# Kernel optimization log

Hardware: AMD Instinct MI355X
Metric: run time of the kernel (lower is better)

The kernel has to match this reference:

```python
import jax, jax.numpy as jnp
import numpy as np

HIDDEN = 2048
NUM_HEADS = 16
HEAD_DIM = HIDDEN // NUM_HEADS


def setup_inputs() -> dict:
    key = jax.random.key(0)
    k1, k2, k3 = jax.random.split(key, 3)
    B, S = 2, 2048
    hidden_states = jax.random.normal(k1, (B, S, HIDDEN), dtype=jnp.float32)
    attention_mask = jnp.zeros((B, 1, 1, S), dtype=jnp.float32)
    W_qkv = jax.random.normal(k2, (HIDDEN, 3 * HIDDEN), dtype=jnp.float32) * (1.0 / np.sqrt(HIDDEN))
    b_qkv = jnp.zeros((3 * HIDDEN,), dtype=jnp.float32)
    W_out = jax.random.normal(k3, (HIDDEN, HIDDEN), dtype=jnp.float32) * (1.0 / np.sqrt(HIDDEN))
    b_out = jnp.zeros((HIDDEN,), dtype=jnp.float32)
    return {"hidden_states": hidden_states, "attention_mask": attention_mask,
            "W_qkv": W_qkv, "b_qkv": b_qkv, "W_out": W_out, "b_out": b_out}


def reference(hidden_states, attention_mask, W_qkv, b_qkv, W_out, b_out):
    B, S, H = hidden_states.shape
    scale = 1.0 / np.sqrt(HEAD_DIM)
    # fused QKV projection (column-parallel linear, world_size=1)
    mixed = hidden_states @ W_qkv + b_qkv                      # [B,S,3H]
    q, k, v = jnp.split(mixed, 3, axis=-1)
    # [B, heads, S, head_dim]
    q = q.reshape(B, S, NUM_HEADS, HEAD_DIM).transpose(0, 2, 1, 3)
    k = k.reshape(B, S, NUM_HEADS, HEAD_DIM).transpose(0, 2, 1, 3)
    v = v.reshape(B, S, NUM_HEADS, HEAD_DIM).transpose(0, 2, 1, 3)
    scores = jnp.einsum('bhqd,bhkd->bhqk', q, k) * scale       # [B,h,S,S]
    scores = scores + attention_mask                            # additive mask broadcast
    probs = jax.nn.softmax(scores, axis=-1)
    ctx = jnp.einsum('bhqk,bhkd->bhqd', probs, v)               # [B,h,S,d]
    ctx = ctx.transpose(0, 2, 1, 3).reshape(B, S, H)
    return ctx @ W_out + b_out
```

## Files before the change

### kernel.cpp

```cpp
#include <hip/hip_runtime.h>
#include <hip/hip_bf16.h>
#include <stdint.h>

typedef __attribute__((ext_vector_type(4)))  float   f32x4;
typedef __attribute__((ext_vector_type(16))) float   f32x16;
typedef __attribute__((ext_vector_type(8)))  __bf16  bf16x8;
typedef __attribute__((ext_vector_type(8)))  short   s16x8;
typedef __attribute__((ext_vector_type(4)))  unsigned short u16x4;
typedef __attribute__((ext_vector_type(4)))  float   fl4;
typedef __attribute__((ext_vector_type(2)))  unsigned int u32x2;
typedef __attribute__((ext_vector_type(4)))  unsigned int u32x4;

#define DEVFN static __device__ __forceinline__

constexpr int BATCH = 2, SEQ = 2048, HID = 2048, NHEAD = 16, HDIM = 128;
constexpr int MROWS = BATCH * SEQ;
constexpr int N3    = 3 * HID;
constexpr float LOG2E = 1.44269504088896340736f;
constexpr float SCALE_LOG2E = 0.12751649736170852f;
constexpr float DEFER_THR = 11.541560327111708f;

DEVFN unsigned short f2bf(float f) {
  unsigned int u = __float_as_uint(f);
  u += 0x7FFFu + ((u >> 16) & 1u);
  return (unsigned short)(u >> 16);
}
DEVFN float bf2f(unsigned short h) { return __uint_as_float(((unsigned int)h) << 16); }

DEVFN void async_cp16(const void* g, void* l) {
  __builtin_amdgcn_global_load_lds(
      (__attribute__((address_space(1))) void*)g,
      (__attribute__((address_space(3))) void*)l, 16, 0, 0);
}

DEVFN f32x4 mfma_bf16(bf16x8 a, bf16x8 b, f32x4 c) {
  return __builtin_amdgcn_mfma_f32_16x16x32_bf16(a, b, c, 0, 0, 0);
}
DEVFN f32x16 mfma32(bf16x8 a, bf16x8 b, f32x16 c) {
  return __builtin_amdgcn_mfma_f32_32x32x16_bf16(a, b, c, 0, 0, 0);
}
DEVFN unsigned cvt_pk_bf16(float lo, float hi) {
  unsigned r;
  asm("v_cvt_pk_bf16_f32 %0, %1, %2" : "=v"(r) : "v"(lo), "v"(hi));
  return r;
}

__global__ __launch_bounds__(256) void cvt_bf16(const float* __restrict__ x,
                                                unsigned short* __restrict__ hi, int n4) {
  for (int i = blockIdx.x * blockDim.x + threadIdx.x; i < n4; i += gridDim.x * blockDim.x) {
    fl4 v = ((const fl4*)x)[i];
    u16x4 h;
#pragma unroll
    for (int j = 0; j < 4; j++) h[j] = f2bf(v[j]);
    ((u16x4*)hi)[i] = h;
  }
}

__global__ __launch_bounds__(256) void cvt_transpose(const float* __restrict__ W,
                                                     unsigned short* __restrict__ T,
                                                     int R, int C) {
  __shared__ float tile[32][33];
  const int c0 = blockIdx.x * 32, r0 = blockIdx.y * 32;
  const int tx = threadIdx.x, ty = threadIdx.y;
#pragma unroll
  for (int i = 0; i < 4; i++) tile[ty + 8 * i][tx] = W[(size_t)(r0 + ty + 8 * i) * C + c0 + tx];
  __syncthreads();
#pragma unroll
  for (int i = 0; i < 4; i++) {
    const float v = tile[tx][ty + 8 * i];
    T[(size_t)(c0 + ty + 8 * i) * R + r0 + tx] = f2bf(v);
  }
}

template <bool OUT_BF16>
__global__ __launch_bounds__(512, 1) void gemm_ring(const unsigned short* __restrict__ A,
                                                    const unsigned short* __restrict__ Bt,
                                                    const float* __restrict__ bias,
                                                    void* __restrict__ Cout, int Ndim) {
  constexpr int KDIM  = 2048;
  constexpr int NT    = KDIM / 64;
  constexpr int ASLOT = 256 * 64;
  constexpr int BSLOT = 128 * 64;
  constexpr int SLOT  = ASLOT + BSLOT;
  __shared__ __align__(16) unsigned short smem[3 * SLOT];

  const int tid = threadIdx.x;
  const int wid = tid >> 6, lane = tid & 63;
  const int wm = wid >> 2, wn = wid & 3;
  const int g = lane >> 4, q = lane & 15;
  const int n0 = blockIdx.x * 128, m0 = blockIdx.y * 256;

  const int srow = (wid << 3) + (lane >> 3);
  const int scol = (((lane & 7) ^ (lane >> 3)) << 4);
  const char* gA = (const char*)A  + ((size_t)(m0 + srow) * KDIM) * 2 + scol;
  const char* gB = (const char*)Bt + ((size_t)(n0 + srow) * KDIM) * 2 + scol;
  const int dbase = ((wid << 3)) << 7;

  f32x4 acc[8][2] = {};
  const int axor = (q & 7) << 4;

  auto STAGE = [&](int tt, int slot) {
    char* sA = (char*)(smem + slot * SLOT);
    char* sB = (char*)(smem + slot * SLOT + ASLOT);
    const size_t koff = (size_t)tt << 7;
#pragma unroll
    for (int i = 0; i < 4; i++)
      async_cp16(gA + (size_t)(i * 64) * (KDIM * 2) + koff, sA + dbase + (i << 13));
#pragma unroll
    for (int i = 0; i < 2; i++)
      async_cp16(gB + (size_t)(i * 64) * (KDIM * 2) + koff, sB + dbase + (i << 13));
  };

  auto COMPUTE = [&](int slot) {
    const char* sA = (const char*)(smem + slot * SLOT);
    const char* sB = (const char*)(smem + slot * SLOT + ASLOT);
#pragma unroll
    for (int ks = 0; ks < 2; ks++) {
      const int kb = (ks << 6) + (g << 4);
      bf16x8 av[8], bv[2];
#pragma unroll
      for (int nf = 0; nf < 2; nf++) {
        const int row = (wn << 5) + (nf << 4) + q;
        bv[nf] = *(const bf16x8*)(sB + (row << 7) + (kb ^ axor));
      }
#pragma unroll
      for (int mf = 0; mf < 8; mf++) {
        const int row = (wm << 7) + (mf << 4) + q;
        av[mf] = *(const bf16x8*)(sA + (row << 7) + (kb ^ axor));
      }
#pragma unroll
      for (int mf = 0; mf < 8; mf++)
#pragma unroll
        for (int nf = 0; nf < 2; nf++)
          acc[mf][nf] = mfma_bf16(av[mf], bv[nf], acc[mf][nf]);
    }
  };

  STAGE(0, 0);
  STAGE(1, 1);
  int s2 = 2, sc = 0;
#pragma unroll 1
  for (int t = 0; t < NT - 2; ++t) {
    asm volatile("s_waitcnt vmcnt(6)" ::: "memory");
    __builtin_amdgcn_s_barrier();
    asm volatile("" ::: "memory");
    STAGE(t + 2, s2);
    COMPUTE(sc);
    s2 = (s2 == 2) ? 0 : s2 + 1;
    sc = (sc == 2) ? 0 : sc + 1;
  }
  asm volatile("s_waitcnt vmcnt(6)" ::: "memory");
  __builtin_amdgcn_s_barrier();
  asm volatile("" ::: "memory");
  COMPUTE(sc);
  sc = (sc == 2) ? 0 : sc + 1;
  asm volatile("s_waitcnt vmcnt(0)" ::: "memory");
  __builtin_amdgcn_s_barrier();
  asm volatile("" ::: "memory");
  COMPUTE(sc);

  float bvv[2];
#pragma unroll
  for (int nf = 0; nf < 2; nf++) bvv[nf] = bias[n0 + (wn << 5) + (nf << 4) + q];
#pragma unroll
  for (int mf = 0; mf < 8; mf++) {
    const int rowg = m0 + (wm << 7) + (mf << 4) + (g << 2);
#pragma unroll
    for (int nf = 0; nf < 2; nf++) {
      const int colg = n0 + (wn << 5) + (nf << 4) + q;
#pragma unroll
      for (int r = 0; r < 4; r++) {
        const float v = acc[mf][nf][r] + bvv[nf];
        if (OUT_BF16)
          ((unsigned short*)Cout)[(size_t)(rowg + r) * Ndim + colg] = f2bf(v);
        else
          ((float*)Cout)[(size_t)(rowg + r) * Ndim + colg] = v;
      }
    }
  }
}

__global__ __launch_bounds__(256) void transpose_v(const unsigned short* __restrict__ qkv,
                                                   unsigned short* __restrict__ vt) {
  __shared__ __align__(16) unsigned short tile[64][136];
  const int z = blockIdx.y, b = z >> 4, h = z & 15;
  const int s0 = blockIdx.x << 6;
  const int t = threadIdx.x;
#pragma unroll
  for (int i = 0; i < 4; i++) {
    const int idx = t + (i << 8);
    const int row = idx >> 4, ch = idx & 15;
    *(s16x8*)&tile[row][ch << 3] =
        *(const s16x8*)(qkv + (size_t)(b * SEQ + s0 + row) * N3 + 2 * HID + h * HDIM + (ch << 3));
  }
  __syncthreads();
#pragma unroll
  for (int i = 0; i < 4; i++) {
    const int idx = t + (i << 8);
    const int d = idx >> 3, sc = idx & 7;
    s16x8 v;
#pragma unroll
    for (int j = 0; j < 8; j++) v[j] = (short)tile[(sc << 3) + j][d];
    *(s16x8*)(vt + (size_t)(z * HDIM + d) * SEQ + s0 + (sc << 3)) = v;
  }
}

__global__ __launch_bounds__(512, 2) void attn_kernel(const unsigned short* __restrict__ qkv,
                                                      const unsigned short* __restrict__ vt,
                                                      const float* __restrict__ mask,
                                                      unsigned short* __restrict__ ctx) {
  constexpr int NT    = SEQ / 64;
  constexpr int KSLOT = 64 * 128;
  constexpr int VSLOT = 128 * 64;
  constexpr int SLOT  = KSLOT + VSLOT;
  __shared__ __align__(16) unsigned short sKV[3 * SLOT];
  __shared__ __align__(16) float sM[SEQ];

  const int bid = blockIdx.x;
  const int z  = ((bid & 7) << 2) + ((bid >> 3) >> 3);
  const int qb = (bid >> 3) & 7;
  const int b = z >> 4, h = z & 15;
  const int tid = threadIdx.x, wid = tid >> 6, lane = tid & 63;
  const int l31 = lane & 31, hi = lane >> 5;
  const int q0w = (qb << 8) + (wid << 5);

  {
    fl4 m = ((const fl4*)(mask + (size_t)b * SEQ))[tid];
    m *= LOG2E;
    ((fl4*)sM)[tid] = m;
  }

  bf16x8 bq[8];
  {
    const char* qrow = (const char*)(qkv + (size_t)(b * SEQ + q0w + l31) * N3 + h * HDIM);
#pragma unroll
    for (int kc = 0; kc < 8; kc++) bq[kc] = *(const bf16x8*)(qrow + (kc << 5) + (hi << 4));
  }

  f32x16 acc2[4] = {};
  float mrun = -1e30f, lrun = 0.f;

  const char* gK = (const char*)qkv + ((size_t)(b * SEQ) * N3 + HID + h * HDIM) * 2;
  const char* gV = (const char*)vt + ((size_t)z * HDIM * SEQ) * 2;

  auto STAGE = [&](int tt, int slot) {
    char* base = (char*)(sKV + slot * SLOT);
    const int k0 = tt << 6;
#pragma unroll
    for (int i = 0; i < 2; i++) {
      const int krow = (i << 5) + (tid >> 4);
      const int kc = (((tid & 15) << 4)) ^ ((krow & 7) << 4);
      async_cp16(gK + ((size_t)(k0 + krow) * N3) * 2 + kc, base + (i << 13) + (wid << 10));
    }
#pragma unroll
    for (int i = 0; i < 2; i++) {
      const int vrow = (i << 6) + (tid >> 3);
      const int vc = (((tid & 7) << 4)) ^ ((vrow & 7) << 4);
      async_cp16(gV + ((size_t)vrow * SEQ + k0) * 2 + vc,
                 base + (KSLOT * 2) + (i << 13) + (wid << 10));
    }
  };

  auto COMPUTE = [&](int t, int slot) {
    const char* sK = (const char*)(sKV + slot * SLOT);
    const char* sV = (const char*)(sKV + slot * SLOT + KSLOT);
    const int k0 = t << 6;

    f32x16 accs[2] = {};
    __builtin_amdgcn_s_setprio(1);
#pragma unroll
    for (int kb = 0; kb < 2; kb++)
#pragma unroll
      for (int kc = 0; kc < 8; kc++) {
        const bf16x8 ka = *(const bf16x8*)(sK + (((kb << 5) + l31) << 8) +
                                           (((kc << 5) + (hi << 4)) ^ ((l31 & 7) << 4)));
        accs[kb] = mfma32(ka, bq[kc], accs[kb]);
      }
    __builtin_amdgcn_s_setprio(0);

    float p_[2][16];
#pragma unroll
    for (int kb = 0; kb < 2; kb++) {
      fl4 mk[4];
#pragma unroll
      for (int m = 0; m < 4; m++) mk[m] = *(const fl4*)&sM[k0 + (kb << 5) + (m << 3) + (hi << 2)];
#pragma unroll
      for (int r = 0; r < 16; r++)
        p_[kb][r] = fmaf(accs[kb][r], SCALE_LOG2E, mk[r >> 2][r & 3]);
    }
    float mt = p_[0][0];
#pragma unroll
    for (int kb = 0; kb < 2; kb++)
#pragma unroll
      for (int r = 0; r < 16; r++) mt = fmaxf(mt, p_[kb][r]);
    mt = fmaxf(mt, __shfl_xor(mt, 32));
    if (!__all(mt <= mrun + DEFER_THR)) {
      const float mnew = fmaxf(mrun, mt);
      const float fs = exp2f(mrun - mnew);
      lrun *= fs;
#pragma unroll
      for (int r = 0; r < 16; r++) {
        const int qr = (r & 3) + ((r >> 2) << 3) + (hi << 2);
        const float fr = __shfl(fs, (lane & 32) | qr);
#pragma unroll
        for (int db = 0; db < 4; db++) acc2[db][r] *= fr;
      }
      mrun = mnew;
    }
    float ps = 0.f;
#pragma unroll
    for (int kb = 0; kb < 2; kb++)
#pragma unroll
      for (int r = 0; r < 16; r++) {
        const float e = exp2f(p_[kb][r] - mrun);
        p_[kb][r] = e;
        ps += e;
      }
    ps += __shfl_xor(ps, 32);
    lrun += ps;

    bf16x8 pa[4];
#pragma unroll
    for (int kb = 0; kb < 2; kb++)
#pragma unroll
      for (int hh = 0; hh < 2; hh++) {
        const float* pp = &p_[kb][hh << 3];
        const unsigned x01 = cvt_pk_bf16(pp[0], pp[1]);
        const unsigned x23 = cvt_pk_bf16(pp[2], pp[3]);
        const unsigned y01 = cvt_pk_bf16(pp[4], pp[5]);
        const unsigned y23 = cvt_pk_bf16(pp[6], pp[7]);
        const u32x2 sa = __builtin_amdgcn_permlane32_swap(x01, y01, false, false);
        const u32x2 sb = __builtin_amdgcn_permlane32_swap(x23, y23, false, false);
        const u32x4 w = {sa[0], sb[0], sa[1], sb[1]};
        pa[(kb << 1) + hh] = __builtin_bit_cast(bf16x8, w);
      }

    __builtin_amdgcn_s_setprio(1);
#pragma unroll
    for (int db = 0; db < 4; db++)
#pragma unroll
      for (int ks = 0; ks < 4; ks++) {
        const bf16x8 bv = *(const bf16x8*)(sV + (((db << 5) + l31) << 7) +
                                           (((ks << 5) + (hi << 4)) ^ ((l31 & 7) << 4)));
        acc2[db] = mfma32(pa[ks], bv, acc2[db]);
      }
    __builtin_amdgcn_s_setprio(0);
  };

  STAGE(0, 0);
  STAGE(1, 1);
  __syncthreads();
  int s2 = 2, sc = 0;
#pragma unroll 1
  for (int t = 0; t < NT - 2; ++t) {
    asm volatile("s_waitcnt vmcnt(4)" ::: "memory");
    __builtin_amdgcn_s_barrier();
    asm volatile("" ::: "memory");
    STAGE(t + 2, s2);
    COMPUTE(t, sc);
    s2 = (s2 == 2) ? 0 : s2 + 1;
    sc = (sc == 2) ? 0 : sc + 1;
  }
  asm volatile("s_waitcnt vmcnt(4)" ::: "memory");
  __builtin_amdgcn_s_barrier();
  asm volatile("" ::: "memory");
  COMPUTE(NT - 2, sc);
  sc = (sc == 2) ? 0 : sc + 1;
  asm volatile("s_waitcnt vmcnt(0)" ::: "memory");
  __builtin_amdgcn_s_barrier();
  asm volatile("" ::: "memory");
  COMPUTE(NT - 1, sc);

  const float inv = 1.f / lrun;
#pragma unroll
  for (int r = 0; r < 16; r++) {
    const int qr = (r & 3) + ((r >> 2) << 3) + (hi << 2);
    const float fr = __shfl(inv, (lane & 32) | qr);
    unsigned short* crow = ctx + (size_t)(b * SEQ + q0w + qr) * HID + h * HDIM + l31;
#pragma unroll
    for (int db = 0; db < 4; db++) crow[db << 5] = f2bf(acc2[db][r] * fr);
  }
}

extern "C" void kernel_launch(void* const* d_in, const int* in_sizes, int n_in,
                              void* d_out, int out_size, void* d_ws, size_t ws_size,
                              hipStream_t stream) {
  const float* hs   = (const float*)d_in[0];
  const float* mask = (const float*)d_in[1];
  const float* Wqkv = (const float*)d_in[2];
  const float* bqkv = (const float*)d_in[3];
  const float* Wout = (const float*)d_in[4];
  const float* bout = (const float*)d_in[5];

  char* ws = (char*)d_ws;
  size_t off = 0;
  auto alloc = [&](size_t n) { char* p = ws + off; off += (n + 255) & ~(size_t)255; return p; };
  unsigned short* hs_bf = (unsigned short*)alloc((size_t)MROWS * HID * 2);
  unsigned short* wq_bf = (unsigned short*)alloc((size_t)N3 * HID * 2);
  unsigned short* wo_bf = (unsigned short*)alloc((size_t)HID * HID * 2);
  unsigned short* qkvb  = (unsigned short*)alloc((size_t)MROWS * N3 * 2);
  unsigned short* vtb   = (unsigned short*)alloc((size_t)BATCH * NHEAD * HDIM * SEQ * 2);
  unsigned short* ctxb  = (unsigned short*)alloc((size_t)MROWS * HID * 2);
  (void)ws_size;

  cvt_bf16<<<2048, 256, 0, stream>>>(hs, hs_bf, MROWS * HID / 4);
  dim3 tb(32, 8);
  cvt_transpose<<<dim3(N3 / 32, HID / 32), tb, 0, stream>>>(Wqkv, wq_bf, HID, N3);
  cvt_transpose<<<dim3(HID / 32, HID / 32), tb, 0, stream>>>(Wout, wo_bf, HID, HID);
  gemm_ring<true ><<<dim3(N3 / 128, MROWS / 256), 512, 0, stream>>>(hs_bf, wq_bf, bqkv, qkvb, N3);
  transpose_v<<<dim3(SEQ / 64, BATCH * NHEAD), 256, 0, stream>>>(qkvb, vtb);
  attn_kernel<<<256, 512, 0, stream>>>(qkvb, vtb, mask, ctxb);
  gemm_ring<false><<<dim3(HID / 128, MROWS / 256), 512, 0, stream>>>(ctxb, wo_bf, bout, (float*)d_out, HID);
}
```

Before: 268.9 us.

## Shrink attention blocks to 4 waves with double-buffered KV and new LDS swizzle

The attention kernel now uses 256-thread blocks covering 128 query rows (512 blocks instead of 256). The 3-slot KV ring becomes a double buffer, and the wait-for-all-loads plus barrier moves to the end of each iteration. The K/V LDS layout is reorganised with a 16-way XOR swizzle, and V is stored as two 64-row halves. The aim is more blocks and lower LDS use per block, so more blocks fit per CU and the tail is balanced better, at the cost of re-reading K/V twice as often and a shallower prefetch pipeline.

```diff
diff --git a/kernel.cpp b/kernel.cpp
--- a/kernel.cpp
+++ b/kernel.cpp
@@ -25,7 +25,6 @@
   u += 0x7FFFu + ((u >> 16) & 1u);
   return (unsigned short)(u >> 16);
 }
-DEVFN float bf2f(unsigned short h) { return __uint_as_float(((unsigned int)h) << 16); }
 
 DEVFN void async_cp16(const void* g, void* l) {
   __builtin_amdgcn_global_load_lds(
@@ -205,29 +204,31 @@
   }
 }
 
-__global__ __launch_bounds__(512, 2) void attn_kernel(const unsigned short* __restrict__ qkv,
+__global__ __launch_bounds__(256, 2) void attn_kernel(const unsigned short* __restrict__ qkv,
                                                       const unsigned short* __restrict__ vt,
                                                       const float* __restrict__ mask,
                                                       unsigned short* __restrict__ ctx) {
   constexpr int NT    = SEQ / 64;
   constexpr int KSLOT = 64 * 128;
-  constexpr int VSLOT = 128 * 64;
+  constexpr int VSLOT = 64 * 128;
   constexpr int SLOT  = KSLOT + VSLOT;
-  __shared__ __align__(16) unsigned short sKV[3 * SLOT];
+  __shared__ __align__(16) unsigned short sKV[2 * SLOT];
   __shared__ __align__(16) float sM[SEQ];
 
   const int bid = blockIdx.x;
-  const int z  = ((bid & 7) << 2) + ((bid >> 3) >> 3);
-  const int qb = (bid >> 3) & 7;
+  const int idx = bid >> 3;
+  const int z  = ((bid & 7) << 2) + (idx >> 4);
+  const int qb = idx & 15;
   const int b = z >> 4, h = z & 15;
   const int tid = threadIdx.x, wid = tid >> 6, lane = tid & 63;
   const int l31 = lane & 31, hi = lane >> 5;
-  const int q0w = (qb << 8) + (wid << 5);
-
-  {
-    fl4 m = ((const fl4*)(mask + (size_t)b * SEQ))[tid];
+  const int q0w = (qb << 7) + (wid << 5);
+
+#pragma unroll
+  for (int j = 0; j < 2; j++) {
+    fl4 m = ((const fl4*)(mask + (size_t)b * SEQ))[tid + (j << 8)];
     m *= LOG2E;
-    ((fl4*)sM)[tid] = m;
+    ((fl4*)sM)[tid + (j << 8)] = m;
   }
 
   bf16x8 bq[8];
@@ -244,20 +245,20 @@
   const char* gV = (const char*)vt + ((size_t)z * HDIM * SEQ) * 2;
 
   auto STAGE = [&](int tt, int slot) {
-    char* base = (char*)(sKV + slot * SLOT);
+    char* kb_ = (char*)(sKV + slot * SLOT);
+    char* vb_ = kb_ + KSLOT * 2;
     const int k0 = tt << 6;
 #pragma unroll
-    for (int i = 0; i < 2; i++) {
-      const int krow = (i << 5) + (tid >> 4);
-      const int kc = (((tid & 15) << 4)) ^ ((krow & 7) << 4);
-      async_cp16(gK + ((size_t)(k0 + krow) * N3) * 2 + kc, base + (i << 13) + (wid << 10));
-    }
-#pragma unroll
-    for (int i = 0; i < 2; i++) {
-      const int vrow = (i << 6) + (tid >> 3);
-      const int vc = (((tid & 7) << 4)) ^ ((vrow & 7) << 4);
-      async_cp16(gV + ((size_t)vrow * SEQ + k0) * 2 + vc,
-                 base + (KSLOT * 2) + (i << 13) + (wid << 10));
+    for (int i = 0; i < 4; i++) {
+      const int row = (i << 4) + (wid << 2) + (lane >> 4);
+      const int sl  = lane & 15;
+      const int dst = (i << 12) + (wid << 10);
+      async_cp16(gK + ((size_t)(k0 + row) * N3) * 2 + (((sl ^ (row & 15))) << 4),
+                 kb_ + dst);
+      const int sv  = sl ^ (row & 15);
+      const int dhi = sv >> 3, kc8 = sv & 7;
+      async_cp16(gV + ((size_t)((dhi << 6) + row) * SEQ + k0 + (kc8 << 3)) * 2,
+                 vb_ + dst);
     }
   };
 
@@ -272,8 +273,9 @@
     for (int kb = 0; kb < 2; kb++)
 #pragma unroll
       for (int kc = 0; kc < 8; kc++) {
-        const bf16x8 ka = *(const bf16x8*)(sK + (((kb << 5) + l31) << 8) +
-                                           (((kc << 5) + (hi << 4)) ^ ((l31 & 7) << 4)));
+        const int key = (kb << 5) + l31;
+        const bf16x8 ka = *(const bf16x8*)(sK + (key << 8) +
+                                           ((((kc << 1) + hi) ^ (l31 & 15)) << 4));
         accs[kb] = mfma32(ka, bq[kc], accs[kb]);
       }
     __builtin_amdgcn_s_setprio(0);
@@ -337,39 +339,29 @@
 
     __builtin_amdgcn_s_setprio(1);
 #pragma unroll
-    for (int db = 0; db < 4; db++)
+    for (int db = 0; db < 4; db++) {
+      const int dd = ((db & 1) << 5) + l31;
 #pragma unroll
       for (int ks = 0; ks < 4; ks++) {
-        const bf16x8 bv = *(const bf16x8*)(sV + (((db << 5) + l31) << 7) +
-                                           (((ks << 5) + (hi << 4)) ^ ((l31 & 7) << 4)));
+        const int sv = ((db >> 1) << 3) + (ks << 1) + hi;
+        const bf16x8 bv = *(const bf16x8*)(sV + (dd << 8) + ((sv ^ (l31 & 15)) << 4));
         acc2[db] = mfma32(pa[ks], bv, acc2[db]);
       }
+    }
     __builtin_amdgcn_s_setprio(0);
   };
 
   STAGE(0, 0);
-  STAGE(1, 1);
   __syncthreads();
-  int s2 = 2, sc = 0;
 #pragma unroll 1
-  for (int t = 0; t < NT - 2; ++t) {
-    asm volatile("s_waitcnt vmcnt(4)" ::: "memory");
+  for (int t = 0; t < NT - 1; ++t) {
+    STAGE(t + 1, (t + 1) & 1);
+    COMPUTE(t, t & 1);
+    asm volatile("s_waitcnt vmcnt(0)" ::: "memory");
     __builtin_amdgcn_s_barrier();
     asm volatile("" ::: "memory");
-    STAGE(t + 2, s2);
-    COMPUTE(t, sc);
-    s2 = (s2 == 2) ? 0 : s2 + 1;
-    sc = (sc == 2) ? 0 : sc + 1;
-  }
-  asm volatile("s_waitcnt vmcnt(4)" ::: "memory");
-  __builtin_amdgcn_s_barrier();
-  asm volatile("" ::: "memory");
-  COMPUTE(NT - 2, sc);
-  sc = (sc == 2) ? 0 : sc + 1;
-  asm volatile("s_waitcnt vmcnt(0)" ::: "memory");
-  __builtin_amdgcn_s_barrier();
-  asm volatile("" ::: "memory");
-  COMPUTE(NT - 1, sc);
+  }
+  COMPUTE(NT - 1, (NT - 1) & 1);
 
   const float inv = 1.f / lrun;
 #pragma unroll
@@ -409,6 +401,6 @@
   cvt_transpose<<<dim3(HID / 32, HID / 32), tb, 0, stream>>>(Wout, wo_bf, HID, HID);
   gemm_ring<true ><<<dim3(N3 / 128, MROWS / 256), 512, 0, stream>>>(hs_bf, wq_bf, bqkv, qkvb, N3);
   transpose_v<<<dim3(SEQ / 64, BATCH * NHEAD), 256, 0, stream>>>(qkvb, vtb);
-  attn_kernel<<<256, 512, 0, stream>>>(qkvb, vtb, mask, ctxb);
+  attn_kernel<<<512, 256, 0, stream>>>(qkvb, vtb, mask, ctxb);
   gemm_ring<false><<<dim3(HID / 128, MROWS / 256), 512, 0, stream>>>(ctxb, wo_bf, bout, (float*)d_out, HID);
 }
```

Result: no change. 267.1 us (-0.7%).
